# Kernel optimization log

Hardware: AMD Instinct MI355X
Metric: run time of the kernel (lower is better)

The kernel has to match this reference:

```python
import jax, jax.numpy as jnp
import numpy as np

B, NPG, K, DIN, DOUT, EMB, HEADS = 64, 1024, 32, 512, 512, 32, 4
HD = EMB // HEADS  # head dim = 8


def layernorm(x, g, b, eps=1e-5):
    m = jnp.mean(x, axis=-1, keepdims=True)
    v = jnp.var(x, axis=-1, keepdims=True)
    return (x - m) / jnp.sqrt(v + eps) * g + b


def _xavier(key, out_f, in_f, gain=0.5):
    std = gain * np.sqrt(2.0 / (in_f + out_f))
    return jax.random.normal(key, (out_f, in_f), dtype=jnp.float32) * std


def setup_inputs() -> dict:
    key = jax.random.key(0)
    ks = jax.random.split(key, 16)
    N = B * NPG
    x = jax.random.normal(ks[0], (N, DIN), dtype=jnp.float32)
    # roughly orthonormal-column scale for eigenvectors
    eigenvectors = jax.random.normal(ks[1], (N, K), dtype=jnp.float32) / np.sqrt(NPG)
    eigenvalues = jax.random.uniform(ks[2], (B * K,), dtype=jnp.float32) * 2.0
    eig_mask = jnp.ones((B * K,), dtype=bool)
    batch = jnp.repeat(jnp.arange(B, dtype=jnp.int64), NPG)
    z = jnp.zeros
    o = jnp.ones
    return {
        "x": x, "eigenvectors": eigenvectors, "eigenvalues": eigenvalues,
        "eig_mask": eig_mask, "batch": batch,
        "W1": _xavier(ks[3], 32, 1), "b1": z(32), "g1": o(32), "be1": z(32),
        "W2": _xavier(ks[4], 32, 32), "b2": z(32), "g2": o(32), "be2": z(32),
        "Wqkv": _xavier(ks[5], 3 * EMB, EMB), "bqkv": z(3 * EMB),
        "Wo": _xavier(ks[6], EMB, EMB), "bo": z(EMB),
        "Wf1": _xavier(ks[7], 64, 32), "bf1": z(64),
        "Wf2": _xavier(ks[8], 1, 64), "bf2": z(1),
        "Wp": _xavier(ks[9], DOUT, DIN), "bp": z(DOUT),
        "gp": o(DOUT), "bep": z(DOUT),
    }


def reference(x, eigenvectors, eigenvalues, eig_mask, batch,
              W1, b1, g1, be1, W2, b2, g2, be2,
              Wqkv, bqkv, Wo, bo, Wf1, bf1, Wf2, bf2, Wp, bp, gp, bep):
    # ---- eigenvalue set encoder (batched over all graphs at once) ----
    ev = eigenvalues.reshape(B, K, 1)                       # [B,K,1]
    h = ev @ W1.T + b1                                      # [B,K,32]
    h = jax.nn.relu(layernorm(h, g1, be1))
    h = layernorm(h @ W2.T + b2, g2, be2)                   # [B,K,32]
    # ---- multi-head self-attention over the K eigenvalues ----
    padding = ~eig_mask.reshape(B, K)                       # True = masked out
    qkv = h @ Wqkv.T + bqkv                                 # [B,K,96]
    q, k_, v = jnp.split(qkv, 3, axis=-1)
    def heads(t):
        return t.reshape(B, K, HEADS, HD).transpose(0, 2, 1, 3)  # [B,H,K,hd]
    q, k_, v = heads(q), heads(k_), heads(v)
    scores = jnp.einsum('bhqd,bhkd->bhqk', q, k_) / np.sqrt(HD)
    scores = jnp.where(padding[:, None, None, :], -1e9, scores)
    attn = jax.nn.softmax(scores, axis=-1)
    ctx = jnp.einsum('bhqk,bhkd->bhqd', attn, v)
    ctx = ctx.transpose(0, 2, 1, 3).reshape(B, K, EMB)
    ctx = ctx @ Wo.T + bo                                   # [B,K,32]
    # ---- filter generator ----
    f = jnp.tanh(jax.nn.relu(ctx @ Wf1.T + bf1) @ Wf2.T + bf2)[..., 0]  # [B,K]
    filters = jnp.where(padding, 0.0, f)
    # ---- spectral filtering per graph (equal-size graphs -> reshape) ----
    xg = x.reshape(B, NPG, DIN)
    vg = eigenvectors.reshape(B, NPG, K)
    x_freq = jnp.einsum('bnk,bnd->bkd', vg, xg)             # U^T x
    x_spat = jnp.einsum('bnk,bkd->bnd', vg, filters[:, :, None] * x_freq)
    out = layernorm(x_spat @ Wp.T + bp, gp, bep)            # [B,NPG,DOUT]
    return out.reshape(B * NPG, DOUT)
```

## Files before the change

kernel.cpp:

```cpp
#include <hip/hip_runtime.h>
#include <math.h>

#define B    64
#define NPG  1024
#define KEIG 32
#define DIN  512
#define DOUT 512
#define NPART 8

typedef float f32x4 __attribute__((ext_vector_type(4)));

__device__ __forceinline__ float rsum32(float v) {
    v += __shfl_xor(v, 1, 32);
    v += __shfl_xor(v, 2, 32);
    v += __shfl_xor(v, 4, 32);
    v += __shfl_xor(v, 8, 32);
    v += __shfl_xor(v, 16, 32);
    return v;
}
__device__ __forceinline__ float rmax32(float v) {
    v = fmaxf(v, __shfl_xor(v, 1, 32));
    v = fmaxf(v, __shfl_xor(v, 2, 32));
    v = fmaxf(v, __shfl_xor(v, 4, 32));
    v = fmaxf(v, __shfl_xor(v, 8, 32));
    v = fmaxf(v, __shfl_xor(v, 16, 32));
    return v;
}
__device__ __forceinline__ float rsum64(float v) {
    v += __shfl_xor(v, 1, 64);
    v += __shfl_xor(v, 2, 64);
    v += __shfl_xor(v, 4, 64);
    v += __shfl_xor(v, 8, 64);
    v += __shfl_xor(v, 16, 64);
    v += __shfl_xor(v, 32, 64);
    return v;
}

__global__ __launch_bounds__(1024) void k1_filters(
    const float* __restrict__ eigenvalues,
    const float* __restrict__ W1,  const float* __restrict__ b1,
    const float* __restrict__ g1,  const float* __restrict__ be1,
    const float* __restrict__ W2,  const float* __restrict__ b2,
    const float* __restrict__ g2,  const float* __restrict__ be2,
    const float* __restrict__ Wqkv,const float* __restrict__ bqkv,
    const float* __restrict__ Wo,  const float* __restrict__ bo,
    const float* __restrict__ Wf1, const float* __restrict__ bf1,
    const float* __restrict__ Wf2, const float* __restrict__ bf2,
    float* __restrict__ filters)
{
    __shared__ float wts[224][33];
    __shared__ float hA[KEIG][33];
    __shared__ float hB[KEIG][33];
    __shared__ float qkv[KEIG][97];
    __shared__ float attn[4 * 1064];

    const int t = threadIdx.x;
    const int k = t >> 5;
    const int j = t & 31;
    const int b = blockIdx.x;

    {
        const int row = t >> 5, i = t & 31;
        wts[row][i]       = W2[t];
        wts[32 + row][i]  = Wqkv[t];
        wts[64 + row][i]  = Wqkv[1024 + t];
        wts[96 + row][i]  = Wqkv[2048 + t];
        wts[128 + row][i] = Wo[t];
        wts[160 + row][i] = Wf1[t];
        wts[192 + row][i] = Wf1[1024 + t];
    }

    const float ev = eigenvalues[b * KEIG + k];
    float h1 = ev * W1[j] + b1[j];
    {
        float m = rsum32(h1) * (1.f / 32.f);
        float d = h1 - m;
        float q = rsum32(d * d);
        float r = rsqrtf(q * (1.f / 32.f) + 1e-5f);
        h1 = fmaxf(d * r * g1[j] + be1[j], 0.f);
    }
    hA[k][j] = h1;
    __syncthreads();

    {
        float a = b2[j];
        #pragma unroll
        for (int i = 0; i < 32; ++i) a += hA[k][i] * wts[j][i];
        float m = rsum32(a) * (1.f / 32.f);
        float d = a - m;
        float q = rsum32(d * d);
        float r = rsqrtf(q * (1.f / 32.f) + 1e-5f);
        hB[k][j] = d * r * g2[j] + be2[j];
    }
    __syncthreads();

    {
        float aq = bqkv[j], ak = bqkv[32 + j], av = bqkv[64 + j];
        #pragma unroll
        for (int i = 0; i < 32; ++i) {
            float hv = hB[k][i];
            aq += hv * wts[32 + j][i];
            ak += hv * wts[64 + j][i];
            av += hv * wts[96 + j][i];
        }
        qkv[k][j]      = aq;
        qkv[k][32 + j] = ak;
        qkv[k][64 + j] = av;
    }
    __syncthreads();

    {
        const float inv = 0.35355339059327373f;
        float sc[4];
        #pragma unroll
        for (int hh = 0; hh < 4; ++hh) {
            float s = 0.f;
            #pragma unroll
            for (int d2 = 0; d2 < 8; ++d2)
                s += qkv[k][hh * 8 + d2] * qkv[j][32 + hh * 8 + d2];
            sc[hh] = s * inv;
        }
        #pragma unroll
        for (int hh = 0; hh < 4; ++hh) {
            float mx  = rmax32(sc[hh]);
            float e   = __expf(sc[hh] - mx);
            float den = rsum32(e);
            attn[hh * 1064 + k * 33 + j] = e / den;
        }
    }
    __syncthreads();

    {
        const int hh = j >> 3;
        float c = 0.f;
        #pragma unroll
        for (int k2 = 0; k2 < 32; ++k2)
            c += attn[hh * 1064 + k * 33 + k2] * qkv[k2][64 + j];
        hA[k][j] = c;
    }
    __syncthreads();

    {
        float o = bo[j];
        #pragma unroll
        for (int i = 0; i < 32; ++i) o += hA[k][i] * wts[128 + j][i];
        hB[k][j] = o;
    }
    __syncthreads();

    {
        float r0 = bf1[j], r1 = bf1[32 + j];
        #pragma unroll
        for (int i = 0; i < 32; ++i) {
            float ov = hB[k][i];
            r0 += ov * wts[160 + j][i];
            r1 += ov * wts[192 + j][i];
        }
        float fp = fmaxf(r0, 0.f) * Wf2[j] + fmaxf(r1, 0.f) * Wf2[32 + j];
        fp = rsum32(fp);
        if (j == 0) filters[b * KEIG + k] = tanhf(fp + bf2[0]);
    }
}

__global__ __launch_bounds__(256) void k2_xfreq_partial(
    const float* __restrict__ x, const float* __restrict__ eigvec,
    float* __restrict__ xfp)
{
    __shared__ float vtile[128][32];
    const int t  = threadIdx.x;
    const int b  = blockIdx.x >> 4;
    const int nc = (blockIdx.x >> 1) & 7;
    const int dh = blockIdx.x & 1;
    const int kq = t >> 6;
    const int ds = t & 63;
    const int d  = dh * 256 + ds * 4;
    const int n0 = nc * 128;

    const float* vb = eigvec + ((size_t)(b * NPG + n0)) * KEIG;
    #pragma unroll
    for (int e = 0; e < 16; ++e) {
        int idx = t + e * 256;
        ((float*)vtile)[idx] = vb[idx];
    }
    __syncthreads();

    float4 acc[8];
    #pragma unroll
    for (int i = 0; i < 8; ++i) acc[i] = make_float4(0.f, 0.f, 0.f, 0.f);

    const float* xb = x + ((size_t)(b * NPG + n0)) * DIN + d;
    #pragma unroll 4
    for (int n = 0; n < 128; ++n) {
        float4 xv = *(const float4*)(xb + (size_t)n * DIN);
        const float4* vp = (const float4*)&vtile[n][kq * 8];
        float4 v0 = vp[0], v1 = vp[1];
        acc[0].x += v0.x * xv.x; acc[0].y += v0.x * xv.y; acc[0].z += v0.x * xv.z; acc[0].w += v0.x * xv.w;
        acc[1].x += v0.y * xv.x; acc[1].y += v0.y * xv.y; acc[1].z += v0.y * xv.z; acc[1].w += v0.y * xv.w;
        acc[2].x += v0.z * xv.x; acc[2].y += v0.z * xv.y; acc[2].z += v0.z * xv.z; acc[2].w += v0.z * xv.w;
        acc[3].x += v0.w * xv.x; acc[3].y += v0.w * xv.y; acc[3].z += v0.w * xv.z; acc[3].w += v0.w * xv.w;
        acc[4].x += v1.x * xv.x; acc[4].y += v1.x * xv.y; acc[4].z += v1.x * xv.z; acc[4].w += v1.x * xv.w;
        acc[5].x += v1.y * xv.x; acc[5].y += v1.y * xv.y; acc[5].z += v1.y * xv.z; acc[5].w += v1.y * xv.w;
        acc[6].x += v1.z * xv.x; acc[6].y += v1.z * xv.y; acc[6].z += v1.z * xv.z; acc[6].w += v1.z * xv.w;
        acc[7].x += v1.w * xv.x; acc[7].y += v1.w * xv.y; acc[7].z += v1.w * xv.z; acc[7].w += v1.w * xv.w;
    }

    #pragma unroll
    for (int kk = 0; kk < 8; ++kk) {
        int kg = kq * 8 + kk;
        *(float4*)(xfp + (((size_t)nc * B + b) * KEIG + kg) * DIN + d) = acc[kk];
    }
}

__global__ __launch_bounds__(256) void k2b_combine(
    const float* __restrict__ xfp, const float* __restrict__ filters,
    float* __restrict__ F)
{
    const int t = threadIdx.x;
    const int m = blockIdx.x * 2 + (t >> 7);
    const int dp = (t & 127) * 4;

    const float* base = xfp + (size_t)m * DIN + dp;
    float4 s = *(const float4*)base;
    #pragma unroll
    for (int q = 1; q < NPART; ++q) {
        float4 sq = *(const float4*)(base + (size_t)q * (B * KEIG * DIN));
        s.x += sq.x; s.y += sq.y; s.z += sq.z; s.w += sq.w;
    }
    const float f = filters[m];
    float4 o = make_float4(s.x * f, s.y * f, s.z * f, s.w * f);
    *(float4*)(F + (size_t)m * DIN + dp) = o;
}

__global__ __launch_bounds__(256) void k3_G(
    const float* __restrict__ F, const float* __restrict__ Wp,
    float* __restrict__ G)
{
    __shared__ float a_lds[64][65];
    __shared__ float b_lds[64][65];

    const int t   = threadIdx.x;
    const int mt  = blockIdx.x >> 3;
    const int ot  = blockIdx.x & 7;
    const int m0  = mt * 64;
    const int o0  = ot * 64;
    const int tr  = t >> 4;
    const int tc  = t & 15;
    const int col4 = tc * 4;

    float acc[4][4] = {{0.f}};

    for (int d0 = 0; d0 < DIN; d0 += 64) {
        __syncthreads();
        #pragma unroll
        for (int p = 0; p < 4; ++p) {
            int r = p * 16 + tr;
            float4 s = *(const float4*)(F + (size_t)(m0 + r) * DIN + d0 + col4);
            a_lds[r][col4 + 0] = s.x;
            a_lds[r][col4 + 1] = s.y;
            a_lds[r][col4 + 2] = s.z;
            a_lds[r][col4 + 3] = s.w;
        }
        #pragma unroll
        for (int p = 0; p < 4; ++p) {
            int r = p * 16 + tr;
            float4 w = *(const float4*)(Wp + (size_t)(o0 + r) * DIN + d0 + col4);
            b_lds[r][col4 + 0] = w.x;
            b_lds[r][col4 + 1] = w.y;
            b_lds[r][col4 + 2] = w.z;
            b_lds[r][col4 + 3] = w.w;
        }
        __syncthreads();
        #pragma unroll 4
        for (int dd = 0; dd < 64; ++dd) {
            float a0 = a_lds[tr * 4 + 0][dd];
            float a1 = a_lds[tr * 4 + 1][dd];
            float a2 = a_lds[tr * 4 + 2][dd];
            float a3 = a_lds[tr * 4 + 3][dd];
            float b0 = b_lds[tc * 4 + 0][dd];
            float b1 = b_lds[tc * 4 + 1][dd];
            float b2 = b_lds[tc * 4 + 2][dd];
            float b3 = b_lds[tc * 4 + 3][dd];
            acc[0][0] += a0 * b0; acc[0][1] += a0 * b1; acc[0][2] += a0 * b2; acc[0][3] += a0 * b3;
            acc[1][0] += a1 * b0; acc[1][1] += a1 * b1; acc[1][2] += a1 * b2; acc[1][3] += a1 * b3;
            acc[2][0] += a2 * b0; acc[2][1] += a2 * b1; acc[2][2] += a2 * b2; acc[2][3] += a2 * b3;
            acc[3][0] += a3 * b0; acc[3][1] += a3 * b1; acc[3][2] += a3 * b2; acc[3][3] += a3 * b3;
        }
    }
    #pragma unroll
    for (int i = 0; i < 4; ++i) {
        float4 v = make_float4(acc[i][0], acc[i][1], acc[i][2], acc[i][3]);
        *(float4*)(G + (size_t)(m0 + tr * 4 + i) * DOUT + o0 + col4) = v;
    }
}

__global__ __launch_bounds__(256) void k4_out(
    const float* __restrict__ eigvec, const float* __restrict__ G,
    const float* __restrict__ bp, const float* __restrict__ gp,
    const float* __restrict__ bep, float* __restrict__ out)
{
    __shared__ float gsh[KEIG][DOUT];
    __shared__ float vgt[KEIG][68];

    const int t  = threadIdx.x;
    const int b  = blockIdx.x >> 4;
    const int n0 = (blockIdx.x & 15) * 64;

    const float4* G4 = (const float4*)(G + (size_t)b * KEIG * DOUT);
    float4* gsh4 = (float4*)gsh;
    #pragma unroll
    for (int e = 0; e < 16; ++e)
        gsh4[t + e * 256] = G4[t + e * 256];

    const float* vb = eigvec + ((size_t)(b * NPG + n0)) * KEIG;
    #pragma unroll
    for (int e = 0; e < 8; ++e) {
        int idx = t + e * 256;
        vgt[idx & 31][idx >> 5] = vb[idx];
    }
    __syncthreads();

    const int w  = t >> 6;
    const int l  = t & 63;
    const int c0 = 4 * l;

    const float4 bpA = *(const float4*)(bp + c0);
    const float4 bpB = *(const float4*)(bp + 256 + c0);
    const float4 gpA = *(const float4*)(gp + c0);
    const float4 gpB = *(const float4*)(gp + 256 + c0);
    const float4 beA = *(const float4*)(bep + c0);
    const float4 beB = *(const float4*)(bep + 256 + c0);

    for (int gq = 0; gq < 4; ++gq) {
        const int rbase = w * 16 + gq * 4;
        float4 aA[4], aB[4];
        #pragma unroll
        for (int r = 0; r < 4; ++r) { aA[r] = bpA; aB[r] = bpB; }

        #pragma unroll 8
        for (int k = 0; k < KEIG; ++k) {
            const float4 ga = *(const float4*)&gsh[k][c0];
            const float4 gb = *(const float4*)&gsh[k][256 + c0];
            const float4 vv = *(const float4*)&vgt[k][rbase];
            const float vr[4] = {vv.x, vv.y, vv.z, vv.w};
            #pragma unroll
            for (int r = 0; r < 4; ++r) {
                aA[r].x += vr[r] * ga.x; aA[r].y += vr[r] * ga.y;
                aA[r].z += vr[r] * ga.z; aA[r].w += vr[r] * ga.w;
                aB[r].x += vr[r] * gb.x; aB[r].y += vr[r] * gb.y;
                aB[r].z += vr[r] * gb.z; aB[r].w += vr[r] * gb.w;
            }
        }

        #pragma unroll
        for (int r = 0; r < 4; ++r) {
            float s = aA[r].x + aA[r].y + aA[r].z + aA[r].w
                    + aB[r].x + aB[r].y + aB[r].z + aB[r].w;
            float q = aA[r].x * aA[r].x + aA[r].y * aA[r].y
                    + aA[r].z * aA[r].z + aA[r].w * aA[r].w
                    + aB[r].x * aB[r].x + aB[r].y * aB[r].y
                    + aB[r].z * aB[r].z + aB[r].w * aB[r].w;
            s = rsum64(s);
            q = rsum64(q);
            float m    = s * (1.f / 512.f);
            float rstd = rsqrtf(q * (1.f / 512.f) - m * m + 1e-5f);

            f32x4 oA, oB;
            oA.x = (aA[r].x - m) * rstd * gpA.x + beA.x;
            oA.y = (aA[r].y - m) * rstd * gpA.y + beA.y;
            oA.z = (aA[r].z - m) * rstd * gpA.z + beA.z;
            oA.w = (aA[r].w - m) * rstd * gpA.w + beA.w;
            oB.x = (aB[r].x - m) * rstd * gpB.x + beB.x;
            oB.y = (aB[r].y - m) * rstd * gpB.y + beB.y;
            oB.z = (aB[r].z - m) * rstd * gpB.z + beB.z;
            oB.w = (aB[r].w - m) * rstd * gpB.w + beB.w;

            size_t row = (size_t)b * NPG + n0 + rbase + r;
            __builtin_nontemporal_store(oA, (f32x4*)(out + row * DOUT + c0));
            __builtin_nontemporal_store(oB, (f32x4*)(out + row * DOUT + 256 + c0));
        }
    }
}

extern "C" void kernel_launch(void* const* d_in, const int* in_sizes, int n_in,
                              void* d_out, int out_size, void* d_ws, size_t ws_size,
                              hipStream_t stream) {
    (void)in_sizes; (void)n_in; (void)out_size; (void)ws_size;
    const float* x    = (const float*)d_in[0];
    const float* vg   = (const float*)d_in[1];
    const float* ev   = (const float*)d_in[2];
    const float* W1   = (const float*)d_in[5];
    const float* b1   = (const float*)d_in[6];
    const float* g1   = (const float*)d_in[7];
    const float* be1  = (const float*)d_in[8];
    const float* W2   = (const float*)d_in[9];
    const float* b2   = (const float*)d_in[10];
    const float* g2   = (const float*)d_in[11];
    const float* be2  = (const float*)d_in[12];
    const float* Wqkv = (const float*)d_in[13];
    const float* bqkv = (const float*)d_in[14];
    const float* Wo   = (const float*)d_in[15];
    const float* bo   = (const float*)d_in[16];
    const float* Wf1  = (const float*)d_in[17];
    const float* bf1  = (const float*)d_in[18];
    const float* Wf2  = (const float*)d_in[19];
    const float* bf2  = (const float*)d_in[20];
    const float* Wp   = (const float*)d_in[21];
    const float* bp   = (const float*)d_in[22];
    const float* gp   = (const float*)d_in[23];
    const float* bep  = (const float*)d_in[24];

    float* outf    = (float*)d_out;
    float* ws      = (float*)d_ws;
    float* filters = ws;
    float* G       = ws + 4096;
    float* xfp     = outf;
    float* F       = outf + 16777216;

    hipLaunchKernelGGL(k1_filters, dim3(B), dim3(1024), 0, stream,
                       ev, W1, b1, g1, be1, W2, b2, g2, be2,
                       Wqkv, bqkv, Wo, bo, Wf1, bf1, Wf2, bf2, filters);
    hipLaunchKernelGGL(k2_xfreq_partial, dim3(B * 16), dim3(256), 0, stream,
                       x, vg, xfp);
    hipLaunchKernelGGL(k2b_combine, dim3(1024), dim3(256), 0, stream,
                       xfp, filters, F);
    hipLaunchKernelGGL(k3_G, dim3(32 * 8), dim3(256), 0, stream,
                       F, Wp, G);
    hipLaunchKernelGGL(k4_out, dim3(B * 16), dim3(256), 0, stream,
                       vg, G, bp, gp, bep, outf);
}
```

Measured before the change: 131.0 us.

## Precompute layernorm row stats via Gram matrix and split output columns

Adds two kernels that compute per-graph Gram statistics of G (G·Gᵀ, row sums, and the dot product with the bias) and then derive each row's layernorm mean and rstd analytically from its eigenvector. This lets k4_out split the 512 output columns across two blocks, which halves LDS per block and doubles the grid, and removes the cross-lane reductions. The cost is two extra launches plus the stats traffic. It also risks precision loss from computing variance as E[x²]−mean² through quadratic forms. Output stores switch from nontemporal to normal stores.

```diff
diff --git a/kernel.cpp b/kernel.cpp
--- a/kernel.cpp
+++ b/kernel.cpp
@@ -24,15 +24,6 @@
     v = fmaxf(v, __shfl_xor(v, 4, 32));
     v = fmaxf(v, __shfl_xor(v, 8, 32));
     v = fmaxf(v, __shfl_xor(v, 16, 32));
-    return v;
-}
-__device__ __forceinline__ float rsum64(float v) {
-    v += __shfl_xor(v, 1, 64);
-    v += __shfl_xor(v, 2, 64);
-    v += __shfl_xor(v, 4, 64);
-    v += __shfl_xor(v, 8, 64);
-    v += __shfl_xor(v, 16, 64);
-    v += __shfl_xor(v, 32, 64);
     return v;
 }
 
@@ -293,90 +284,187 @@
     }
 }
 
+__global__ __launch_bounds__(256) void k3s_stats(
+    const float* __restrict__ G, const float* __restrict__ bp,
+    float* __restrict__ stats)
+{
+    __shared__ float gs[32][68];
+    __shared__ float bps[64];
+    const int b  = blockIdx.x >> 3;
+    const int sl = blockIdx.x & 7;
+    const int o0 = sl * 64;
+    const int t  = threadIdx.x;
+
+    #pragma unroll
+    for (int e = 0; e < 2; ++e) {
+        int fi = t + e * 256;
+        int k  = fi >> 4;
+        int c4 = fi & 15;
+        float4 g = *(const float4*)(G + ((size_t)(b * KEIG + k)) * DOUT + o0 + c4 * 4);
+        *(float4*)&gs[k][c4 * 4] = g;
+    }
+    if (t < 64) bps[t] = bp[o0 + t];
+    __syncthreads();
+
+    const int i0 = t >> 3;
+    const int j0 = t & 7;
+    float m0 = 0.f, m1 = 0.f, m2 = 0.f, m3 = 0.f, gm = 0.f, cc = 0.f;
+    #pragma unroll 8
+    for (int o = 0; o < 64; ++o) {
+        int oe = (o + i0) & 63;
+        float gi = gs[i0][oe];
+        m0 = fmaf(gi, gs[j0][oe],      m0);
+        m1 = fmaf(gi, gs[j0 + 8][oe],  m1);
+        m2 = fmaf(gi, gs[j0 + 16][oe], m2);
+        m3 = fmaf(gi, gs[j0 + 24][oe], m3);
+        gm += gi;
+        cc = fmaf(gi, bps[oe], cc);
+    }
+    float* Sb = stats + (size_t)(b * 8 + sl) * 1152;
+    Sb[i0 * 32 + j0]      = m0;
+    Sb[i0 * 32 + j0 + 8]  = m1;
+    Sb[i0 * 32 + j0 + 16] = m2;
+    Sb[i0 * 32 + j0 + 24] = m3;
+    if (j0 == 0) { Sb[1024 + i0] = gm; Sb[1056 + i0] = cc; }
+    if (t == 0) {
+        float s1 = 0.f, s2 = 0.f;
+        for (int o = 0; o < 64; ++o) { float v = bps[o]; s1 += v; s2 += v * v; }
+        Sb[1088] = s1; Sb[1089] = s2;
+    }
+}
+
+__global__ __launch_bounds__(256) void k3r_rowstats(
+    const float* __restrict__ eigvec, const float* __restrict__ stats,
+    float2* __restrict__ rowstats)
+{
+    __shared__ float Ms[1090];
+    const int b  = blockIdx.x >> 2;
+    const int rc = blockIdx.x & 3;
+    const int t  = threadIdx.x;
+
+    for (int e = t; e < 1090; e += 256) {
+        float s = 0.f;
+        #pragma unroll
+        for (int sl = 0; sl < 8; ++sl)
+            s += stats[(size_t)(b * 8 + sl) * 1152 + e];
+        Ms[e] = s * (1.f / 512.f);
+    }
+    __syncthreads();
+
+    const int n = b * NPG + rc * 256 + t;
+    const float* vr = eigvec + (size_t)n * KEIG;
+    float v[32];
+    #pragma unroll
+    for (int e = 0; e < 8; ++e) {
+        float4 vv = *(const float4*)(vr + e * 4);
+        v[e * 4 + 0] = vv.x; v[e * 4 + 1] = vv.y;
+        v[e * 4 + 2] = vv.z; v[e * 4 + 3] = vv.w;
+    }
+    float qf = 0.f, mean = 0.f, vc = 0.f;
+    #pragma unroll
+    for (int i = 0; i < 32; ++i) {
+        float mi = 0.f;
+        #pragma unroll
+        for (int j4 = 0; j4 < 8; ++j4) {
+            float4 mr = *(const float4*)&Ms[i * 32 + j4 * 4];
+            mi = fmaf(mr.x, v[j4 * 4 + 0], mi);
+            mi = fmaf(mr.y, v[j4 * 4 + 1], mi);
+            mi = fmaf(mr.z, v[j4 * 4 + 2], mi);
+            mi = fmaf(mr.w, v[j4 * 4 + 3], mi);
+        }
+        qf = fmaf(v[i], mi, qf);
+    }
+    #pragma unroll
+    for (int i4 = 0; i4 < 8; ++i4) {
+        float4 gm = *(const float4*)&Ms[1024 + i4 * 4];
+        float4 cv = *(const float4*)&Ms[1056 + i4 * 4];
+        mean = fmaf(gm.x, v[i4 * 4 + 0], mean);
+        mean = fmaf(gm.y, v[i4 * 4 + 1], mean);
+        mean = fmaf(gm.z, v[i4 * 4 + 2], mean);
+        mean = fmaf(gm.w, v[i4 * 4 + 3], mean);
+        vc   = fmaf(cv.x, v[i4 * 4 + 0], vc);
+        vc   = fmaf(cv.y, v[i4 * 4 + 1], vc);
+        vc   = fmaf(cv.z, v[i4 * 4 + 2], vc);
+        vc   = fmaf(cv.w, v[i4 * 4 + 3], vc);
+    }
+    mean += Ms[1088];
+    float e2  = qf + 2.f * vc + Ms[1089];
+    float var = e2 - mean * mean;
+    rowstats[n] = make_float2(mean, rsqrtf(var + 1e-5f));
+}
+
 __global__ __launch_bounds__(256) void k4_out(
     const float* __restrict__ eigvec, const float* __restrict__ G,
+    const float2* __restrict__ rowstats,
     const float* __restrict__ bp, const float* __restrict__ gp,
     const float* __restrict__ bep, float* __restrict__ out)
 {
-    __shared__ float gsh[KEIG][DOUT];
+    __shared__ float gsh[KEIG][256];
     __shared__ float vgt[KEIG][68];
-
-    const int t  = threadIdx.x;
-    const int b  = blockIdx.x >> 4;
-    const int n0 = (blockIdx.x & 15) * 64;
-
-    const float4* G4 = (const float4*)(G + (size_t)b * KEIG * DOUT);
-    float4* gsh4 = (float4*)gsh;
-    #pragma unroll
-    for (int e = 0; e < 16; ++e)
-        gsh4[t + e * 256] = G4[t + e * 256];
-
+    __shared__ float2 rsh[64];
+
+    const int t    = threadIdx.x;
+    const int b    = blockIdx.x >> 5;
+    const int rc   = (blockIdx.x >> 1) & 15;
+    const int half = blockIdx.x & 1;
+    const int n0   = rc * 64;
+    const int hc0  = half * 256;
+
+    #pragma unroll
+    for (int e = 0; e < 8; ++e) {
+        int fi = t + e * 256;
+        int k  = fi >> 6;
+        int c4 = fi & 63;
+        float4 g = *(const float4*)(G + ((size_t)(b * KEIG + k)) * DOUT + hc0 + c4 * 4);
+        *(float4*)&gsh[k][c4 * 4] = g;
+    }
     const float* vb = eigvec + ((size_t)(b * NPG + n0)) * KEIG;
     #pragma unroll
     for (int e = 0; e < 8; ++e) {
         int idx = t + e * 256;
         vgt[idx & 31][idx >> 5] = vb[idx];
     }
+    if (t < 64) rsh[t] = rowstats[b * NPG + n0 + t];
     __syncthreads();
 
     const int w  = t >> 6;
     const int l  = t & 63;
     const int c0 = 4 * l;
 
-    const float4 bpA = *(const float4*)(bp + c0);
-    const float4 bpB = *(const float4*)(bp + 256 + c0);
-    const float4 gpA = *(const float4*)(gp + c0);
-    const float4 gpB = *(const float4*)(gp + 256 + c0);
-    const float4 beA = *(const float4*)(bep + c0);
-    const float4 beB = *(const float4*)(bep + 256 + c0);
+    const float4 bpv = *(const float4*)(bp + hc0 + c0);
+    const float4 gpv = *(const float4*)(gp + hc0 + c0);
+    const float4 bev = *(const float4*)(bep + hc0 + c0);
 
     for (int gq = 0; gq < 4; ++gq) {
         const int rbase = w * 16 + gq * 4;
-        float4 aA[4], aB[4];
-        #pragma unroll
-        for (int r = 0; r < 4; ++r) { aA[r] = bpA; aB[r] = bpB; }
+        float4 aa[4];
+        #pragma unroll
+        for (int r = 0; r < 4; ++r) aa[r] = bpv;
 
         #pragma unroll 8
         for (int k = 0; k < KEIG; ++k) {
-            const float4 ga = *(const float4*)&gsh[k][c0];
-            const float4 gb = *(const float4*)&gsh[k][256 + c0];
+            const float4 g  = *(const float4*)&gsh[k][c0];
             const float4 vv = *(const float4*)&vgt[k][rbase];
             const float vr[4] = {vv.x, vv.y, vv.z, vv.w};
             #pragma unroll
             for (int r = 0; r < 4; ++r) {
-                aA[r].x += vr[r] * ga.x; aA[r].y += vr[r] * ga.y;
-                aA[r].z += vr[r] * ga.z; aA[r].w += vr[r] * ga.w;
-                aB[r].x += vr[r] * gb.x; aB[r].y += vr[r] * gb.y;
-                aB[r].z += vr[r] * gb.z; aB[r].w += vr[r] * gb.w;
+                aa[r].x = fmaf(vr[r], g.x, aa[r].x);
+                aa[r].y = fmaf(vr[r], g.y, aa[r].y);
+                aa[r].z = fmaf(vr[r], g.z, aa[r].z);
+                aa[r].w = fmaf(vr[r], g.w, aa[r].w);
             }
         }
 
         #pragma unroll
         for (int r = 0; r < 4; ++r) {
-            float s = aA[r].x + aA[r].y + aA[r].z + aA[r].w
-                    + aB[r].x + aB[r].y + aB[r].z + aB[r].w;
-            float q = aA[r].x * aA[r].x + aA[r].y * aA[r].y
-                    + aA[r].z * aA[r].z + aA[r].w * aA[r].w
-                    + aB[r].x * aB[r].x + aB[r].y * aB[r].y
-                    + aB[r].z * aB[r].z + aB[r].w * aB[r].w;
-            s = rsum64(s);
-            q = rsum64(q);
-            float m    = s * (1.f / 512.f);
-            float rstd = rsqrtf(q * (1.f / 512.f) - m * m + 1e-5f);
-
-            f32x4 oA, oB;
-            oA.x = (aA[r].x - m) * rstd * gpA.x + beA.x;
-            oA.y = (aA[r].y - m) * rstd * gpA.y + beA.y;
-            oA.z = (aA[r].z - m) * rstd * gpA.z + beA.z;
-            oA.w = (aA[r].w - m) * rstd * gpA.w + beA.w;
-            oB.x = (aB[r].x - m) * rstd * gpB.x + beB.x;
-            oB.y = (aB[r].y - m) * rstd * gpB.y + beB.y;
-            oB.z = (aB[r].z - m) * rstd * gpB.z + beB.z;
-            oB.w = (aB[r].w - m) * rstd * gpB.w + beB.w;
-
+            float2 ms = rsh[rbase + r];
+            float4 o4;
+            o4.x = (aa[r].x - ms.x) * ms.y * gpv.x + bev.x;
+            o4.y = (aa[r].y - ms.x) * ms.y * gpv.y + bev.y;
+            o4.z = (aa[r].z - ms.x) * ms.y * gpv.z + bev.z;
+            o4.w = (aa[r].w - ms.x) * ms.y * gpv.w + bev.w;
             size_t row = (size_t)b * NPG + n0 + rbase + r;
-            __builtin_nontemporal_store(oA, (f32x4*)(out + row * DOUT + c0));
-            __builtin_nontemporal_store(oB, (f32x4*)(out + row * DOUT + 256 + c0));
+            *(float4*)(out + row * DOUT + hc0 + c0) = o4;
         }
     }
 }
@@ -413,6 +501,8 @@
     float* ws      = (float*)d_ws;
     float* filters = ws;
     float* G       = ws + 4096;
+    float* stats   = ws + 4096 + 1048576;
+    float2* rowst  = (float2*)(ws + 4096 + 1048576 + 589824);
     float* xfp     = outf;
     float* F       = outf + 16777216;
 
@@ -425,6 +515,10 @@
                        xfp, filters, F);
     hipLaunchKernelGGL(k3_G, dim3(32 * 8), dim3(256), 0, stream,
                        F, Wp, G);
-    hipLaunchKernelGGL(k4_out, dim3(B * 16), dim3(256), 0, stream,
-                       vg, G, bp, gp, bep, outf);
-}
+    hipLaunchKernelGGL(k3s_stats, dim3(B * 8), dim3(256), 0, stream,
+                       G, bp, stats);
+    hipLaunchKernelGGL(k3r_rowstats, dim3(B * 4), dim3(256), 0, stream,
+                       vg, stats, rowst);
+    hipLaunchKernelGGL(k4_out, dim3(B * 32), dim3(256), 0, stream,
+                       vg, G, rowst, bp, gp, bep, outf);
+}
```

Result: slower. 152.8 us (+16.7%).
